# Kernel tuning notes

Measured on AMD Instinct MI355X. Metric: run time of the kernel, lower is better.

Reference implementation:

```python
import jax, jax.numpy as jnp
import numpy as np

B, C, H, W, K, O, KS = 32, 16, 256, 256, 4, 16, 3
C4 = C // 4


def setup_inputs() -> dict:
    key = jax.random.key(0)
    ks = jax.random.split(key, 6)
    return {
        "x": jax.random.normal(ks[0], (B, C, H, W), dtype=jnp.float32),
        "weight": jax.random.normal(ks[1], (K, O, C, KS, KS), dtype=jnp.float32),
        "attn_w1": jax.random.normal(ks[2], (C4, C), dtype=jnp.float32) * 0.1,
        "attn_b1": jnp.zeros((C4,), dtype=jnp.float32),
        "attn_w2": jax.random.normal(ks[3], (K, C4), dtype=jnp.float32) * 0.1,
        "attn_b2": jnp.zeros((K,), dtype=jnp.float32),
    }


def reference(x, weight, attn_w1, attn_b1, attn_w2, attn_b2):
    # Attention branch: global avg pool -> 1x1 conv -> relu -> 1x1 conv -> softmax over K
    pooled = x.mean(axis=(2, 3))                                  # (B, C)
    h = jax.nn.relu(pooled @ attn_w1.T + attn_b1)                 # (B, C//4)
    attn = jax.nn.softmax(h @ attn_w2.T + attn_b2, axis=1)        # (B, K)

    # Per-sample aggregated kernel: sum_k attn[b,k] * weight[k]
    agg_w = jnp.einsum('bk,koihw->boihw', attn, weight)           # (B, O, C, KS, KS)

    # Per-sample conv2d (equivalent to torch grouped conv with groups=B)
    pad = ((1, 1), (1, 1))
    def per_sample(xi, wi):
        # xi: (C, H, W), wi: (O, C, KS, KS)
        return jax.lax.conv_general_dilated(
            xi[None], wi, window_strides=(1, 1), padding=pad,
            dimension_numbers=('NCHW', 'OIHW', 'NCHW'))[0]
    return jax.vmap(per_sample)(x, agg_w)                         # (B, O, H, W)
```

## Files before the change

### kernel.cpp

```cpp
#include <hip/hip_runtime.h>

#define BD  32
#define CD  16
#define HD  256
#define WD  256
#define KD  4
#define OD  16
#define C4D 4

__device__ float g_pooled[BD * CD];
__device__ float g_agg[BD * CD * 9 * OD];

__global__ void pool_kernel(const float* __restrict__ x) {
    const int plane = blockIdx.x;
    const float4* xp4 = reinterpret_cast<const float4*>(x + (size_t)plane * (HD * WD));

    float s = 0.f;
    #pragma unroll 4
    for (int j = threadIdx.x; j < HD * WD / 4; j += 256) {
        float4 v = xp4[j];
        s += v.x + v.y + v.z + v.w;
    }

    __shared__ float red[256];
    red[threadIdx.x] = s;
    __syncthreads();
    for (int off = 128; off > 0; off >>= 1) {
        if (threadIdx.x < off) red[threadIdx.x] += red[threadIdx.x + off];
        __syncthreads();
    }
    if (threadIdx.x == 0) g_pooled[plane] = red[0];
}

__global__ void attn_agg_kernel(const float* __restrict__ w1, const float* __restrict__ b1,
                                const float* __restrict__ w2, const float* __restrict__ b2,
                                const float* __restrict__ weight) {
    const int b = blockIdx.x;

    float p[CD];
    #pragma unroll
    for (int c = 0; c < CD; ++c) p[c] = g_pooled[b * CD + c] * (1.f / (HD * WD));

    float h[C4D];
    #pragma unroll
    for (int j = 0; j < C4D; ++j) {
        float s = b1[j];
        #pragma unroll
        for (int c = 0; c < CD; ++c) s = fmaf(p[c], w1[j * CD + c], s);
        h[j] = fmaxf(s, 0.f);
    }

    float lg[KD];
    float mx = -1e30f;
    #pragma unroll
    for (int k = 0; k < KD; ++k) {
        float s = b2[k];
        #pragma unroll
        for (int j = 0; j < C4D; ++j) s = fmaf(h[j], w2[k * C4D + j], s);
        lg[k] = s;
        mx = fmaxf(mx, s);
    }
    float se = 0.f;
    #pragma unroll
    for (int k = 0; k < KD; ++k) { lg[k] = expf(lg[k] - mx); se += lg[k]; }
    const float inv = 1.f / se;

    for (int idx = threadIdx.x; idx < CD * 9 * OD; idx += 256) {
        const int o   = idx & 15;
        const int t   = idx >> 4;
        const int c   = t / 9;
        const int tap = t - c * 9;
        float s = 0.f;
        #pragma unroll
        for (int k = 0; k < KD; ++k)
            s = fmaf(lg[k] * inv, weight[((k * OD + o) * CD + c) * 9 + tap], s);
        g_agg[b * (CD * 9 * OD) + idx] = s;
    }
}

__global__ __launch_bounds__(256, 2)
void conv_kernel(const float* __restrict__ x, float* __restrict__ out) {
    const int strip = blockIdx.x;
    const int b     = blockIdx.y;
    const int ct    = threadIdx.x;
    const int r0    = strip * 8;

    __shared__ float xlds[4][10][264];
    __shared__ float wlds[CD * 9 * OD];

    {
        const float* wb = g_agg + b * (CD * 9 * OD);
        for (int i = threadIdx.x; i < CD * 9 * OD; i += 256) wlds[i] = wb[i];
    }
    if (threadIdx.x < 80) {
        const int ch  = threadIdx.x / 20;
        const int rem = threadIdx.x % 20;
        xlds[ch][rem >> 1][(rem & 1) ? 260 : 3] = 0.f;
    }

    float acc[8][OD];
    #pragma unroll
    for (int r = 0; r < 8; ++r)
        #pragma unroll
        for (int o = 0; o < OD; ++o) acc[r][o] = 0.f;

    float4 pre[10];

    #define STAGE_LOAD(gg)                                                       \
        _Pragma("unroll")                                                        \
        for (int i = 0; i < 10; ++i) {                                           \
            const int idx = threadIdx.x + i * 256;                               \
            const int ch  = idx / 640;                                           \
            const int rem = idx - ch * 640;                                      \
            const int rr  = rem >> 6;                                            \
            const int j   = rem & 63;                                            \
            const int row = r0 - 1 + rr;                                         \
            pre[i] = make_float4(0.f, 0.f, 0.f, 0.f);                            \
            if (row >= 0 && row < HD)                                            \
                pre[i] = *reinterpret_cast<const float4*>(                       \
                    x + (size_t)(b * CD + (gg) * 4 + ch) * (HD * WD)             \
                      + row * WD + 4 * j);                                       \
        }

    #define STAGE_WRITE()                                                        \
        _Pragma("unroll")                                                        \
        for (int i = 0; i < 10; ++i) {                                           \
            const int idx = threadIdx.x + i * 256;                               \
            const int ch  = idx / 640;                                           \
            const int rem = idx - ch * 640;                                      \
            const int rr  = rem >> 6;                                            \
            const int j   = rem & 63;                                            \
            *reinterpret_cast<float4*>(&xlds[ch][rr][4 + 4 * j]) = pre[i];       \
        }

    STAGE_LOAD(0)
    STAGE_WRITE()
    __syncthreads();

    #pragma unroll 1
    for (int g = 0; g < 4; ++g) {
        if (g < 3) STAGE_LOAD(g + 1)

        #pragma unroll 1
        for (int ch = 0; ch < 4; ++ch) {
            float xw[10][3];
            #pragma unroll
            for (int rr = 0; rr < 10; ++rr)
                #pragma unroll
                for (int kk = 0; kk < 3; ++kk)
                    xw[rr][kk] = xlds[ch][rr][ct + 3 + kk];

            const float4* wc4 = reinterpret_cast<const float4*>(&wlds[(g * 4 + ch) * 144]);
            #pragma unroll
            for (int ky = 0; ky < 3; ++ky)
                #pragma unroll
                for (int kx = 0; kx < 3; ++kx)
                    #pragma unroll
                    for (int o4 = 0; o4 < 4; ++o4) {
                        const float4 w4 = wc4[(ky * 3 + kx) * 4 + o4];
                        #pragma unroll
                        for (int r = 0; r < 8; ++r) {
                            const float xv = xw[r + ky][kx];
                            acc[r][4 * o4 + 0] = fmaf(w4.x, xv, acc[r][4 * o4 + 0]);
                            acc[r][4 * o4 + 1] = fmaf(w4.y, xv, acc[r][4 * o4 + 1]);
                            acc[r][4 * o4 + 2] = fmaf(w4.z, xv, acc[r][4 * o4 + 2]);
                            acc[r][4 * o4 + 3] = fmaf(w4.w, xv, acc[r][4 * o4 + 3]);
                        }
                    }
        }
        __syncthreads();
        if (g < 3) {
            STAGE_WRITE()
            __syncthreads();
        }
    }
    #undef STAGE_LOAD
    #undef STAGE_WRITE

    #pragma unroll
    for (int o = 0; o < OD; ++o)
        #pragma unroll
        for (int r = 0; r < 8; ++r)
            out[(((size_t)b * OD + o) * HD + (r0 + r)) * WD + ct] = acc[r][o];
}

extern "C" void kernel_launch(void* const* d_in, const int* in_sizes, int n_in,
                              void* d_out, int out_size, void* d_ws, size_t ws_size,
                              hipStream_t stream) {
    (void)in_sizes; (void)n_in; (void)out_size; (void)d_ws; (void)ws_size;
    const float* x      = (const float*)d_in[0];
    const float* weight = (const float*)d_in[1];
    const float* w1     = (const float*)d_in[2];
    const float* b1     = (const float*)d_in[3];
    const float* w2     = (const float*)d_in[4];
    const float* b2     = (const float*)d_in[5];
    float* out = (float*)d_out;

    pool_kernel<<<512, 256, 0, stream>>>(x);
    attn_agg_kernel<<<32, 256, 0, stream>>>(w1, b1, w2, b2, weight);
    conv_kernel<<<dim3(32, 32), 256, 0, stream>>>(x, out);
}
```

Measured before the change: 369.2 us.

## Halve conv strip height, drop register prefetch, raise occupancy to three blocks

The conv kernel now computes 4 output rows per block instead of 8, doubling the grid to 64 strips per sample. The halo tile shrinks to 6 rows and the accumulator array is halved. The register-staged prefetch of the next channel group is removed in favour of direct global-to-LDS loads after the barrier. Launch bounds ask for 3 blocks per SIMD group. Together these lower register and LDS pressure to allow more concurrent waves. In exchange, the 2-row halo is now reloaded relative to 4 rows instead of 8, and the loads of the next group no longer overlap with compute.

```diff
diff --git a/kernel.cpp b/kernel.cpp
--- a/kernel.cpp
+++ b/kernel.cpp
@@ -78,74 +78,59 @@
     }
 }
 
-__global__ __launch_bounds__(256, 2)
+__global__ __launch_bounds__(256, 3)
 void conv_kernel(const float* __restrict__ x, float* __restrict__ out) {
     const int strip = blockIdx.x;
     const int b     = blockIdx.y;
     const int ct    = threadIdx.x;
-    const int r0    = strip * 8;
+    const int r0    = strip * 4;
 
-    __shared__ float xlds[4][10][264];
+    __shared__ float xlds[4][6][264];
     __shared__ float wlds[CD * 9 * OD];
 
     {
         const float* wb = g_agg + b * (CD * 9 * OD);
         for (int i = threadIdx.x; i < CD * 9 * OD; i += 256) wlds[i] = wb[i];
     }
-    if (threadIdx.x < 80) {
-        const int ch  = threadIdx.x / 20;
-        const int rem = threadIdx.x % 20;
+    if (threadIdx.x < 48) {
+        const int ch  = threadIdx.x / 12;
+        const int rem = threadIdx.x % 12;
         xlds[ch][rem >> 1][(rem & 1) ? 260 : 3] = 0.f;
     }
 
-    float acc[8][OD];
+    float acc[4][OD];
     #pragma unroll
-    for (int r = 0; r < 8; ++r)
+    for (int r = 0; r < 4; ++r)
         #pragma unroll
         for (int o = 0; o < OD; ++o) acc[r][o] = 0.f;
 
-    float4 pre[10];
-
-    #define STAGE_LOAD(gg)                                                       \
+    #define STAGE(gg)                                                            \
         _Pragma("unroll")                                                        \
-        for (int i = 0; i < 10; ++i) {                                           \
-            const int idx = threadIdx.x + i * 256;                               \
-            const int ch  = idx / 640;                                           \
-            const int rem = idx - ch * 640;                                      \
-            const int rr  = rem >> 6;                                            \
-            const int j   = rem & 63;                                            \
-            const int row = r0 - 1 + rr;                                         \
-            pre[i] = make_float4(0.f, 0.f, 0.f, 0.f);                            \
+        for (int i = 0; i < 6; ++i) {                                            \
+            const int idx    = threadIdx.x + i * 256;                            \
+            const int rowIdx = idx >> 6;                              \
+            const int j      = idx & 63;                                         \
+            const int ch     = rowIdx / 6;                                       \
+            const int rr     = rowIdx - ch * 6;                                  \
+            const int row    = r0 - 1 + rr;                                      \
+            float4 v = make_float4(0.f, 0.f, 0.f, 0.f);                          \
             if (row >= 0 && row < HD)                                            \
-                pre[i] = *reinterpret_cast<const float4*>(                       \
+                v = *reinterpret_cast<const float4*>(                            \
                     x + (size_t)(b * CD + (gg) * 4 + ch) * (HD * WD)             \
                       + row * WD + 4 * j);                                       \
+            *reinterpret_cast<float4*>(&xlds[ch][rr][4 + 4 * j]) = v;            \
         }
 
-    #define STAGE_WRITE()                                                        \
-        _Pragma("unroll")                                                        \
-        for (int i = 0; i < 10; ++i) {                                           \
-            const int idx = threadIdx.x + i * 256;                               \
-            const int ch  = idx / 640;                                           \
-            const int rem = idx - ch * 640;                                      \
-            const int rr  = rem >> 6;                                            \
-            const int j   = rem & 63;                                            \
-            *reinterpret_cast<float4*>(&xlds[ch][rr][4 + 4 * j]) = pre[i];       \
-        }
-
-    STAGE_LOAD(0)
-    STAGE_WRITE()
+    STAGE(0)
     __syncthreads();
 
     #pragma unroll 1
     for (int g = 0; g < 4; ++g) {
-        if (g < 3) STAGE_LOAD(g + 1)
-
         #pragma unroll 1
         for (int ch = 0; ch < 4; ++ch) {
-            float xw[10][3];
+            float xw[6][3];
             #pragma unroll
-            for (int rr = 0; rr < 10; ++rr)
+            for (int rr = 0; rr < 6; ++rr)
                 #pragma unroll
                 for (int kk = 0; kk < 3; ++kk)
                     xw[rr][kk] = xlds[ch][rr][ct + 3 + kk];
@@ -159,7 +144,7 @@
                     for (int o4 = 0; o4 < 4; ++o4) {
                         const float4 w4 = wc4[(ky * 3 + kx) * 4 + o4];
                         #pragma unroll
-                        for (int r = 0; r < 8; ++r) {
+                        for (int r = 0; r < 4; ++r) {
                             const float xv = xw[r + ky][kx];
                             acc[r][4 * o4 + 0] = fmaf(w4.x, xv, acc[r][4 * o4 + 0]);
                             acc[r][4 * o4 + 1] = fmaf(w4.y, xv, acc[r][4 * o4 + 1]);
@@ -170,17 +155,16 @@
         }
         __syncthreads();
         if (g < 3) {
-            STAGE_WRITE()
+            STAGE(g + 1)
             __syncthreads();
         }
     }
-    #undef STAGE_LOAD
-    #undef STAGE_WRITE
+    #undef STAGE
 
     #pragma unroll
     for (int o = 0; o < OD; ++o)
         #pragma unroll
-        for (int r = 0; r < 8; ++r)
+        for (int r = 0; r < 4; ++r)
             out[(((size_t)b * OD + o) * HD + (r0 + r)) * WD + ct] = acc[r][o];
 }
 
@@ -198,5 +182,5 @@
 
     pool_kernel<<<512, 256, 0, stream>>>(x);
     attn_agg_kernel<<<32, 256, 0, stream>>>(w1, b1, w2, b2, weight);
-    conv_kernel<<<dim3(32, 32), 256, 0, stream>>>(x, out);
+    conv_kernel<<<dim3(64, 32), 256, 0, stream>>>(x, out);
 }
```

After: 336.7 us. -8.8%, faster.
